# Kernel tuning notes

Measured on AMD Instinct MI355X. Metric: run time of the kernel, lower is better.

The kernel has to match this reference:

```python
import jax, jax.numpy as jnp
import numpy as np

# Multi-scale deformable attention encoder (Mask2Former pixel decoder transformer)
SHAPES = ((64, 64), (32, 32), (16, 16))  # (H, W) per level, strides 8/16/32 of 512x512
HEADS, POINTS, DM = 8, 4, 256
HD = DM // HEADS
NLVL = len(SHAPES)
NLAYERS = 6
STARTS = np.concatenate([[0], np.cumsum([h * w for h, w in SHAPES])])


def layer_norm(x, g, b, eps=1e-5):
    m = x.mean(-1, keepdims=True)
    v = ((x - m) ** 2).mean(-1, keepdims=True)
    return (x - m) * jax.lax.rsqrt(v + eps) * g + b


def ref_points(B, dtype):
    # valid_ratios == 1 (masks are all-False in the module)
    pts = []
    for H, W in SHAPES:
        ys = (jnp.arange(H, dtype=dtype) + 0.5) / H
        xs = (jnp.arange(W, dtype=dtype) + 0.5) / W
        gy, gx = jnp.meshgrid(ys, xs, indexing='ij')
        pts.append(jnp.stack([gx.reshape(-1), gy.reshape(-1)], -1))
    ref = jnp.concatenate(pts, 0)  # [Q,2]
    return jnp.broadcast_to(ref[None, :, None, :], (B, ref.shape[0], NLVL, 2))


def bilinear(value, loc, H, W):
    # grid_sample(align_corners=False, padding_mode='zeros')
    # value: [B,heads,H*W,d]; loc: [B,Q,heads,P,2] normalized to [0,1]
    x = loc[..., 0] * W - 0.5
    y = loc[..., 1] * H - 0.5
    x0f = jnp.floor(x); y0f = jnp.floor(y)
    lx = x - x0f; ly = y - y0f
    x0 = x0f.astype(jnp.int32); y0 = y0f.astype(jnp.int32)
    out = 0.
    for dx, dy, w in ((0, 0, (1 - lx) * (1 - ly)), (1, 0, lx * (1 - ly)),
                      (0, 1, (1 - lx) * ly), (1, 1, lx * ly)):
        xi = x0 + dx; yi = y0 + dy
        valid = (xi >= 0) & (xi < W) & (yi >= 0) & (yi < H)
        idx = jnp.clip(yi, 0, H - 1) * W + jnp.clip(xi, 0, W - 1)  # [B,Q,heads,P]
        idx_t = jnp.transpose(idx, (0, 2, 1, 3))  # [B,heads,Q,P]
        Bq, hq, Qq, Pq = idx_t.shape
        g = jnp.take_along_axis(value, idx_t.reshape(Bq, hq, Qq * Pq, 1), axis=2)
        g = g.reshape(Bq, hq, Qq, Pq, HD)
        wv = (w * valid).transpose(0, 2, 1, 3)[..., None]  # [B,heads,Q,P,1]
        out = out + g * wv
    return out  # [B,heads,Q,P,d]


def msda(query, src, ref, p):
    off_w, off_b, aw_w, aw_b, val_w, val_b, out_w, out_b = p
    B, Q, _ = query.shape
    value = (src @ val_w.T + val_b).reshape(B, Q, HEADS, HD).transpose(0, 2, 1, 3)  # [B,h,Q,d]
    off = (query @ off_w.T + off_b).reshape(B, Q, HEADS, NLVL, POINTS, 2)
    aw = (query @ aw_w.T + aw_b).reshape(B, Q, HEADS, NLVL * POINTS)
    aw = jax.nn.softmax(aw, -1).reshape(B, Q, HEADS, NLVL, POINTS)
    norm = jnp.array([[W, H] for H, W in SHAPES], dtype=query.dtype)  # [L,2] as (W,H)
    loc = ref[:, :, None, :, None, :] + off / norm[None, None, None, :, None, :]
    samp = []
    for l, (H, W) in enumerate(SHAPES):
        v = value[:, :, STARTS[l]:STARTS[l + 1], :]
        samp.append(bilinear(v, loc[:, :, :, l], H, W))  # [B,h,Q,P,d]
    samp = jnp.stack(samp, 3)  # [B,h,Q,L,P,d]
    w = aw.transpose(0, 2, 1, 3, 4)[..., None]  # [B,h,Q,L,P,1]
    o = (samp * w).sum((3, 4)).transpose(0, 2, 1, 3).reshape(B, Q, DM)
    return o @ out_w.T + out_b


def reference(src0, src1, src2, pos0, pos1, pos2, level_embed,
              off_w, off_b, aw_w, aw_b, val_w, val_b, out_w, out_b,
              ln1_g, ln1_b, ffn1_w, ffn1_b, ffn2_w, ffn2_b, ln2_g, ln2_b):
    srcs, poss = [src0, src1, src2], [pos0, pos1, pos2]
    B = src0.shape[0]
    xs, ps = [], []
    for l, (s, pe) in enumerate(zip(srcs, poss)):
        b, c, h, w = s.shape
        xs.append(s.reshape(b, c, h * w).transpose(0, 2, 1))
        ps.append(pe.reshape(b, c, h * w).transpose(0, 2, 1) + level_embed[l])
    x = jnp.concatenate(xs, 1)    # [B,Q,C]
    pos = jnp.concatenate(ps, 1)  # [B,Q,C]
    ref = ref_points(B, x.dtype)
    for i in range(NLAYERS):
        q = x + pos
        attn = msda(q, x, ref, (off_w[i], off_b[i], aw_w[i], aw_b[i],
                                val_w[i], val_b[i], out_w[i], out_b[i]))
        x = layer_norm(x + attn, ln1_g[i], ln1_b[i])
        h = jax.nn.relu(x @ ffn1_w[i].T + ffn1_b[i])
        x = layer_norm(x + h @ ffn2_w[i].T + ffn2_b[i], ln2_g[i], ln2_b[i])
    return x  # memory [B,Q,C]


def setup_inputs() -> dict:
    key = jax.random.key(0)
    ks = jax.random.split(key, 16)
    s = 0.02
    inp = {}
    inp['src0'] = jax.random.normal(ks[0], (4, 256, 64, 64), jnp.float32)
    inp['src1'] = jax.random.normal(ks[1], (4, 256, 32, 32), jnp.float32)
    inp['src2'] = jax.random.normal(ks[2], (4, 256, 16, 16), jnp.float32)
    inp['pos0'] = jax.random.normal(ks[3], (4, 256, 64, 64), jnp.float32)
    inp['pos1'] = jax.random.normal(ks[4], (4, 256, 32, 32), jnp.float32)
    inp['pos2'] = jax.random.normal(ks[5], (4, 256, 16, 16), jnp.float32)
    inp['level_embed'] = jax.random.normal(ks[6], (3, 256), jnp.float32)
    inp['off_w'] = jax.random.normal(ks[7], (6, 192, 256), jnp.float32) * s
    inp['off_b'] = jnp.zeros((6, 192), jnp.float32)
    inp['aw_w'] = jax.random.normal(ks[8], (6, 96, 256), jnp.float32) * s
    inp['aw_b'] = jnp.zeros((6, 96), jnp.float32)
    inp['val_w'] = jax.random.normal(ks[9], (6, 256, 256), jnp.float32) * s
    inp['val_b'] = jnp.zeros((6, 256), jnp.float32)
    inp['out_w'] = jax.random.normal(ks[10], (6, 256, 256), jnp.float32) * s
    inp['out_b'] = jnp.zeros((6, 256), jnp.float32)
    inp['ln1_g'] = jnp.ones((6, 256), jnp.float32)
    inp['ln1_b'] = jnp.zeros((6, 256), jnp.float32)
    inp['ffn1_w'] = jax.random.normal(ks[11], (6, 1024, 256), jnp.float32) * s
    inp['ffn1_b'] = jnp.zeros((6, 1024), jnp.float32)
    inp['ffn2_w'] = jax.random.normal(ks[12], (6, 256, 1024), jnp.float32) * s
    inp['ffn2_b'] = jnp.zeros((6, 256), jnp.float32)
    inp['ln2_g'] = jnp.ones((6, 256), jnp.float32)
    inp['ln2_b'] = jnp.zeros((6, 256), jnp.float32)
    return inp
```

## Files before the change

### kernel.cpp

```cpp
#include <hip/hip_runtime.h>
#include <hip/hip_bf16.h>
#include <math.h>

#define BB 4
#define QTOT 5376
#define DMM 256
#define NHEADS 8
#define HDIM 32
#define NPTS 4
#define NLVLS 3
#define BQ (BB*QTOT)
#define NOA 288

typedef short bf16x8 __attribute__((ext_vector_type(8)));
typedef unsigned short u16x8 __attribute__((ext_vector_type(8)));
typedef float f32x4  __attribute__((ext_vector_type(4)));

__device__ __forceinline__ unsigned short f2b(float f) {
  unsigned int u = __float_as_uint(f);
  unsigned int r = (u + 0x7FFFu + ((u >> 16) & 1u)) >> 16;
  return (unsigned short)r;
}
__device__ __forceinline__ float b2f(unsigned short u) {
  return __uint_as_float(((unsigned int)u) << 16);
}
__device__ __forceinline__ ushort4 f2b4(float4 v) {
  ushort4 o; o.x = f2b(v.x); o.y = f2b(v.y); o.z = f2b(v.z); o.w = f2b(v.w);
  return o;
}

__device__ __forceinline__ void gload16(const void* g, void* l) {
  __builtin_amdgcn_global_load_lds(
      (const __attribute__((address_space(1))) void*)g,
      (__attribute__((address_space(3))) void*)l, 16, 0, 0);
}

__global__ __launch_bounds__(256) void transpose_in(
    const float* __restrict__ src, const float* __restrict__ emb,
    float* __restrict__ dst, int HW, int qstart)
{
  __shared__ float t[32][33];
  int hw0 = blockIdx.x * 32, c0 = blockIdx.y * 32, b = blockIdx.z;
  int tx = threadIdx.x, ty = threadIdx.y;
  const float* s = src + ((size_t)b * DMM + c0) * HW + hw0;
#pragma unroll
  for (int j = 0; j < 4; j++)
    t[ty * 4 + j][tx] = s[(size_t)(ty * 4 + j) * HW + tx];
  __syncthreads();
  float e = emb ? emb[c0 + tx] : 0.0f;
  float* d = dst + ((size_t)b * QTOT + qstart + hw0) * DMM + c0;
#pragma unroll
  for (int j = 0; j < 4; j++)
    d[(size_t)(ty * 4 + j) * DMM + tx] = t[tx][ty * 4 + j] + e;
}

__global__ __launch_bounds__(256) void conv_b(
    const float* __restrict__ s, unsigned short* __restrict__ d, int n4)
{
  int i = blockIdx.x * 256 + threadIdx.x;
  if (i >= n4) return;
  ((ushort4*)d)[i] = f2b4(((const float4*)s)[i]);
}

__global__ __launch_bounds__(256) void pack_oa(
    const float* __restrict__ offw, const float* __restrict__ aww,
    unsigned short* __restrict__ dst)
{
  int i = blockIdx.x * 256 + threadIdx.x;
  if (i >= 6 * NOA * 64) return;
  int c4 = i & 63;
  int row = (i >> 6) % NOA;
  int l = i / (NOA * 64);
  const float* src = (row < 192)
      ? offw + ((size_t)l * 192 + row) * 256
      : aww  + ((size_t)l * 96 + (row - 192)) * 256;
  float4 v = ((const float4*)src)[c4];
  ((ushort4*)dst)[i] = f2b4(v);
}

__global__ __launch_bounds__(256) void pack_oa_bias(
    const float* __restrict__ offb, const float* __restrict__ awb,
    float* __restrict__ dst)
{
  int i = blockIdx.x * 256 + threadIdx.x;
  if (i >= 6 * NOA) return;
  int row = i % NOA, l = i / NOA;
  dst[i] = (row < 192) ? offb[l * 192 + row] : awb[l * 96 + (row - 192)];
}

__global__ __launch_bounds__(256) void prep(
    const float* __restrict__ x, const float* __restrict__ pos,
    unsigned short* __restrict__ xb, unsigned short* __restrict__ qb,
    unsigned short* __restrict__ pos16, int n4)
{
  int i = blockIdx.x * 256 + threadIdx.x;
  if (i >= n4) return;
  float4 a = ((const float4*)x)[i];
  float4 p = ((const float4*)pos)[i];
  ((ushort4*)xb)[i] = f2b4(a);
  ((ushort4*)pos16)[i] = f2b4(p);
  float4 q = make_float4(a.x + p.x, a.y + p.y, a.z + p.z, a.w + p.w);
  ((ushort4*)qb)[i] = f2b4(q);
}

__device__ __forceinline__ void gemm_tile_body(
    const unsigned short* __restrict__ A, const unsigned short* __restrict__ W,
    int m0, int n0, int K,
    unsigned short (*As)[32], unsigned short (*Ws)[32], f32x4 acc[4][4])
{
  int tid = threadIdx.x;
  int wave = tid >> 6, lane = tid & 63;
  int lr = lane & 15;
  int lkr = ((lane >> 4) ^ (lane & 3)) * 8;
  int wrr = (wave >> 1) * 64;
  int wcc = (wave & 1) * 64;

  int srow = lane >> 2;
  int schunk = ((lane & 3) ^ (srow & 3)) * 8;
  const unsigned short* Ag = A + (size_t)(m0 + wave * 32 + srow) * K + schunk;
  const unsigned short* Wg = W + (size_t)(n0 + wave * 32 + srow) * K + schunk;

#define STAGE_BF(k0, buf)                                                      \
  { int bo = (buf) * 128 + wave * 32;                                          \
    gload16(Ag + (k0), &As[bo][0]);                                            \
    gload16(Ag + (size_t)16 * K + (k0), &As[bo + 16][0]);                      \
    gload16(Wg + (k0), &Ws[bo][0]);                                            \
    gload16(Wg + (size_t)16 * K + (k0), &Ws[bo + 16][0]); }

  STAGE_BF(0, 0);
  __syncthreads();
  int cur = 0;
  for (int k0 = 0; k0 < K; k0 += 32) {
    if (k0 + 32 < K) STAGE_BF(k0 + 32, cur ^ 1);
    int bo = cur * 128;
    bf16x8 af[4], bfv[4];
#pragma unroll
    for (int m = 0; m < 4; m++)
      af[m] = *(const bf16x8*)&As[bo + wrr + m * 16 + lr][lkr];
#pragma unroll
    for (int n = 0; n < 4; n++)
      bfv[n] = *(const bf16x8*)&Ws[bo + wcc + n * 16 + lr][lkr];
#pragma unroll
    for (int m = 0; m < 4; m++)
#pragma unroll
      for (int n = 0; n < 4; n++)
        acc[m][n] = __builtin_amdgcn_mfma_f32_16x16x32_bf16(af[m], bfv[n], acc[m][n], 0, 0, 0);
    __syncthreads();
    cur ^= 1;
  }
#undef STAGE_BF
}

__device__ __forceinline__ void gemm_epilogue(
    const float* __restrict__ bias, void* __restrict__ Cout,
    int m0, int n0, int N, int relu, int bfout, f32x4 acc[4][4])
{
  int tid = threadIdx.x;
  int wave = tid >> 6, lane = tid & 63;
  int lr = lane & 15;
  int wrr = (wave >> 1) * 64;
  int wcc = (wave & 1) * 64;
  float* C32 = (float*)Cout;
  unsigned short* C16 = (unsigned short*)Cout;
#pragma unroll
  for (int n = 0; n < 4; n++) {
    int col = n0 + wcc + n * 16 + lr;
    if (col >= N) continue;
    float bv = bias[col];
#pragma unroll
    for (int m = 0; m < 4; m++) {
      int row0 = m0 + wrr + m * 16 + (lane >> 4) * 4;
#pragma unroll
      for (int j = 0; j < 4; j++) {
        float v = acc[m][n][j] + bv;
        if (relu) v = fmaxf(v, 0.0f);
        if (bfout) C16[(size_t)(row0 + j) * N + col] = f2b(v);
        else       C32[(size_t)(row0 + j) * N + col] = v;
      }
    }
  }
}

__global__ __launch_bounds__(256) void gemm_bf(
    const unsigned short* __restrict__ A, const unsigned short* __restrict__ W,
    const float* __restrict__ bias, void* __restrict__ Cout,
    int M, int N, int K, int flags)
{
  __shared__ unsigned short As[256][32];
  __shared__ unsigned short Ws[256][32];
  f32x4 acc[4][4] = {};
  int m0 = blockIdx.x * 128, n0 = blockIdx.y * 128;
  gemm_tile_body(A, W, m0, n0, K, As, Ws, acc);
  gemm_epilogue(bias, Cout, m0, n0, N, flags & 1, flags & 2, acc);
}

__global__ __launch_bounds__(256) void gemm_valoa(
    const unsigned short* __restrict__ xb, const unsigned short* __restrict__ qb,
    const unsigned short* __restrict__ vW, const unsigned short* __restrict__ oaW,
    const float* __restrict__ vBias, const float* __restrict__ oaBias,
    unsigned short* __restrict__ valb16, unsigned short* __restrict__ offaw16)
{
  __shared__ unsigned short As[256][32];
  __shared__ unsigned short Ws[256][32];
  f32x4 acc[4][4] = {};
  int m0 = blockIdx.x * 128;
  int by = blockIdx.y;
  const int K = 256;
  if (by < 2) {
    int n0 = by * 128;
    gemm_tile_body(xb, vW, m0, n0, K, As, Ws, acc);
    gemm_epilogue(vBias, valb16, m0, n0, 256, 0, 2, acc);
  } else {
    int n0 = (by - 2) * 128;
    gemm_tile_body(qb, oaW, m0, n0, K, As, Ws, acc);
    gemm_epilogue(oaBias, offaw16, m0, n0, NOA, 0, 2, acc);
  }
}

__global__ __launch_bounds__(512) void gemm_ln(
    const unsigned short* __restrict__ A, const unsigned short* __restrict__ W,
    const float* __restrict__ bias, const float* __restrict__ g,
    const float* __restrict__ beta, float* __restrict__ x,
    unsigned short* __restrict__ xb, const unsigned short* __restrict__ pos16,
    unsigned short* __restrict__ qb, int K)
{
  __shared__ unsigned short As[64][32];
  __shared__ unsigned short Ws[512][32];

  int m0 = blockIdx.x * 32;
  int tid = threadIdx.x;
  int wave = tid >> 6, lane = tid & 63;
  int lr = lane & 15;
  int lkr = ((lane >> 4) ^ (lane & 3)) * 8;
  int srow = lane >> 2;
  int schunk = ((lane & 3) ^ (srow & 3)) * 8;

  const unsigned short* Ag = A + (size_t)(m0 + (wave & 1) * 16 + srow) * K + schunk;
  const unsigned short* Wg = W + (size_t)(wave * 32 + srow) * K + schunk;

#define STAGE_LN(k0, buf)                                                      \
  { if (wave < 2) gload16(Ag + (k0), &As[(buf) * 32 + wave * 16][0]);          \
    gload16(Wg + (k0),                  &Ws[(buf) * 256 + wave * 32][0]);      \
    gload16(Wg + (size_t)16 * K + (k0), &Ws[(buf) * 256 + wave * 32 + 16][0]); }

  f32x4 acc[2][2] = {};

  STAGE_LN(0, 0);
  __syncthreads();
  int cur = 0;
  for (int k0 = 0; k0 < K; k0 += 32) {
    if (k0 + 32 < K) STAGE_LN(k0 + 32, cur ^ 1);
    bf16x8 af[2], bfv[2];
#pragma unroll
    for (int m = 0; m < 2; m++)
      af[m] = *(const bf16x8*)&As[cur * 32 + m * 16 + lr][lkr];
#pragma unroll
    for (int n = 0; n < 2; n++)
      bfv[n] = *(const bf16x8*)&Ws[cur * 256 + wave * 32 + n * 16 + lr][lkr];
#pragma unroll
    for (int m = 0; m < 2; m++)
#pragma unroll
      for (int n = 0; n < 2; n++)
        acc[m][n] = __builtin_amdgcn_mfma_f32_16x16x32_bf16(af[m], bfv[n], acc[m][n], 0, 0, 0);
    __syncthreads();
    cur ^= 1;
  }
#undef STAGE_LN

#pragma unroll
  for (int n = 0; n < 2; n++) {
    int col = wave * 32 + n * 16 + lr;
    float bv = bias[col];
#pragma unroll
    for (int m = 0; m < 2; m++) {
      int grow = m0 + m * 16 + (lane >> 4) * 4;
#pragma unroll
      for (int j = 0; j < 4; j++)
        acc[m][n][j] += bv + x[(size_t)(grow + j) * DMM + col];
    }
  }

  float2* red = (float2*)&As[0][0];
#pragma unroll
  for (int m = 0; m < 2; m++) {
#pragma unroll
    for (int j = 0; j < 4; j++) {
      float s  = acc[m][0][j] + acc[m][1][j];
      float s2 = acc[m][0][j] * acc[m][0][j] + acc[m][1][j] * acc[m][1][j];
#pragma unroll
      for (int o = 1; o < 16; o <<= 1) {
        s  += __shfl_xor(s,  o, 64);
        s2 += __shfl_xor(s2, o, 64);
      }
      if (lr == 0)
        red[(m * 16 + (lane >> 4) * 4 + j) * 8 + wave] = make_float2(s, s2);
    }
  }
  __syncthreads();

#pragma unroll
  for (int m = 0; m < 2; m++) {
#pragma unroll
    for (int j = 0; j < 4; j++) {
      int rl = m * 16 + (lane >> 4) * 4 + j;
      float ts = 0.f, ts2 = 0.f;
#pragma unroll
      for (int wv = 0; wv < 8; wv++) {
        float2 r = red[rl * 8 + wv];
        ts += r.x; ts2 += r.y;
      }
      float mean = ts * (1.0f / DMM);
      float var  = ts2 * (1.0f / DMM) - mean * mean;
      float sc = rsqrtf(var + 1e-5f);
      int grow = m0 + rl;
#pragma unroll
      for (int n = 0; n < 2; n++) {
        int col = wave * 32 + n * 16 + lr;
        float o = (acc[m][n][j] - mean) * sc * g[col] + beta[col];
        size_t idx = (size_t)grow * DMM + col;
        x[idx]  = o;
        xb[idx] = f2b(o);
        if (qb) qb[idx] = f2b(o + b2f(pos16[idx]));
      }
    }
  }
}

__global__ __launch_bounds__(256) void msda_sample(
    const unsigned short* __restrict__ value, const unsigned short* __restrict__ offaw16,
    unsigned short* __restrict__ attn16)
{
  __shared__ float saw[8][96];
  __shared__ float smx[64], sinv[64];
  __shared__ float swgt[768 * 4];
  __shared__ int   sofs[768 * 4];

  int tid = threadIdx.x;
  int qi = tid >> 5, t32 = tid & 31;
  int h = t32 >> 2, dg = t32 & 3;
  int bq0 = blockIdx.x * 8;
  int bq = bq0 + qi;
  int b = bq / QTOT;

  for (int i = t32; i < 96; i += 32)
    saw[qi][i] = b2f(offaw16[(size_t)bq * NOA + 192 + i]);
  __syncthreads();

  if (tid < 64) {
    int q2 = tid >> 3, h2 = tid & 7;
    float mx = -1e30f;
#pragma unroll
    for (int t = 0; t < 12; t++) mx = fmaxf(mx, saw[q2][h2 * 12 + t]);
    float den = 0.f;
#pragma unroll
    for (int t = 0; t < 12; t++) den += __expf(saw[q2][h2 * 12 + t] - mx);
    smx[tid] = mx;
    sinv[tid] = 1.0f / den;
  }
  __syncthreads();

  for (int s = tid; s < 768; s += 256) {
    int p = s >> 6;
    int qh = s & 63;
    int q2 = qh >> 3, h2 = qh & 7;
    int l = p >> 2;
    int Wl = 64 >> l;
    int st = (l == 0) ? 0 : ((l == 1) ? 4096 : 5120);

    int q = (bq0 + q2) % QTOT;
    int qq, Wq;
    if (q < 4096)      { qq = q;        Wq = 64; }
    else if (q < 5120) { qq = q - 4096; Wq = 32; }
    else               { qq = q - 5120; Wq = 16; }
    float refx = ((qq % Wq) + 0.5f) / Wq;
    float refy = ((qq / Wq) + 0.5f) / Wq;

    int oi = ((h2 * NLVLS + l) * NPTS + (p & 3)) * 2;
    ushort2 ob = *(const ushort2*)&offaw16[(size_t)(bq0 + q2) * NOA + oi];
    float offx = b2f(ob.x), offy = b2f(ob.y);
    float invW = 1.0f / (float)Wl;
    float xf = (refx + offx * invW) * Wl - 0.5f;
    float yf = (refy + offy * invW) * Wl - 0.5f;
    float x0f = floorf(xf), y0f = floorf(yf);
    float fx = xf - x0f, fy = yf - y0f;
    int x0 = (int)x0f, y0 = (int)y0f;

    float aw = __expf(saw[q2][h2 * 12 + p] - smx[qh]) * sinv[qh];
    float w00 = (1.f - fx) * (1.f - fy) * aw;
    float w10 = fx * (1.f - fy) * aw;
    float w01 = (1.f - fx) * fy * aw;
    float w11 = fx * fy * aw;

    bool xv0 = (x0 >= 0) & (x0 < Wl);
    bool xv1 = (x0 + 1 >= 0) & (x0 + 1 < Wl);
    bool yv0 = (y0 >= 0) & (y0 < Wl);
    bool yv1 = (y0 + 1 >= 0) & (y0 + 1 < Wl);

    int base = s * 4;
    swgt[base + 0] = (xv0 & yv0) ? w00 : 0.f;
    swgt[base + 1] = (xv1 & yv0) ? w10 : 0.f;
    swgt[base + 2] = (xv0 & yv1) ? w01 : 0.f;
    swgt[base + 3] = (xv1 & yv1) ? w11 : 0.f;
    sofs[base + 0] = (xv0 & yv0) ? (st + y0 * Wl + x0) * (DMM * 2) : 0;
    sofs[base + 1] = (xv1 & yv0) ? (st + y0 * Wl + x0 + 1) * (DMM * 2) : 0;
    sofs[base + 2] = (xv0 & yv1) ? (st + (y0 + 1) * Wl + x0) * (DMM * 2) : 0;
    sofs[base + 3] = (xv1 & yv1) ? (st + (y0 + 1) * Wl + x0 + 1) * (DMM * 2) : 0;
  }
  __syncthreads();

  float a8[8];
#pragma unroll
  for (int k = 0; k < 8; k++) a8[k] = 0.f;
  const char* vbase = (const char*)(value + (size_t)b * QTOT * DMM + h * HDIM + dg * 8);
#pragma unroll
  for (int p = 0; p < 12; p++) {
    int s3 = (p * 64 + qi * 8 + h) * 4;
    float4 w = *(const float4*)&swgt[s3];
    int4  of = *(const int4*)&sofs[s3];
    u16x8 g0 = *(const u16x8*)(vbase + of.x);
    u16x8 g1 = *(const u16x8*)(vbase + of.y);
    u16x8 g2 = *(const u16x8*)(vbase + of.z);
    u16x8 g3 = *(const u16x8*)(vbase + of.w);
#pragma unroll
    for (int k = 0; k < 8; k++)
      a8[k] += w.x * b2f((unsigned short)g0[k]) + w.y * b2f((unsigned short)g1[k])
             + w.z * b2f((unsigned short)g2[k]) + w.w * b2f((unsigned short)g3[k]);
  }
  u16x8 o;
#pragma unroll
  for (int k = 0; k < 8; k++) o[k] = f2b(a8[k]);
  *(u16x8*)(attn16 + (size_t)bq * DMM + h * HDIM + dg * 8) = o;
}

extern "C" void kernel_launch(void* const* d_in, const int* in_sizes, int n_in,
                              void* d_out, int out_size, void* d_ws, size_t ws_size,
                              hipStream_t stream)
{
  const float* src[3] = {(const float*)d_in[0], (const float*)d_in[1], (const float*)d_in[2]};
  const float* pin[3] = {(const float*)d_in[3], (const float*)d_in[4], (const float*)d_in[5]};
  const float* lvl_emb = (const float*)d_in[6];
  const float* off_w = (const float*)d_in[7];
  const float* off_b = (const float*)d_in[8];
  const float* aw_w  = (const float*)d_in[9];
  const float* aw_b  = (const float*)d_in[10];
  const float* val_w = (const float*)d_in[11];
  const float* val_b = (const float*)d_in[12];
  const float* out_w = (const float*)d_in[13];
  const float* out_b = (const float*)d_in[14];
  const float* ln1_g = (const float*)d_in[15];
  const float* ln1_b = (const float*)d_in[16];
  const float* ffn1_w = (const float*)d_in[17];
  const float* ffn1_b = (const float*)d_in[18];
  const float* ffn2_w = (const float*)d_in[19];
  const float* ffn2_b = (const float*)d_in[20];
  const float* ln2_g = (const float*)d_in[21];
  const float* ln2_b = (const float*)d_in[22];

  float* x = (float*)d_out;

  char* wsp = (char*)d_ws;
  unsigned short* offaw16 = (unsigned short*)wsp; wsp += (size_t)BQ * NOA * 2;
  unsigned short* valb16  = (unsigned short*)wsp; wsp += (size_t)BQ * 256 * 2;
  unsigned short* attnb   = (unsigned short*)wsp; wsp += (size_t)BQ * 256 * 2;
  unsigned short* hb = offaw16;
  wsp += (size_t)10 * 1024 * 1024;
  float* posb = (float*)wsp;  wsp += (size_t)BQ * 256 * 4;
  unsigned short* pos16 = (unsigned short*)wsp; wsp += (size_t)BQ * 256 * 2;
  unsigned short* xb = (unsigned short*)wsp; wsp += (size_t)BQ * 256 * 2;
  unsigned short* qb = (unsigned short*)wsp; wsp += (size_t)BQ * 256 * 2;

  unsigned short* vWb  = (unsigned short*)wsp; wsp += (size_t)6 * 256 * 256 * 2;
  unsigned short* oaWb = (unsigned short*)wsp; wsp += (size_t)6 * NOA * 256 * 2;
  unsigned short* uWb  = (unsigned short*)wsp; wsp += (size_t)6 * 256 * 256 * 2;
  unsigned short* f1Wb = (unsigned short*)wsp; wsp += (size_t)6 * 1024 * 256 * 2;
  unsigned short* f2Wb = (unsigned short*)wsp; wsp += (size_t)6 * 256 * 1024 * 2;
  float* oaBias = (float*)wsp; wsp += (size_t)6 * NOA * 4;
  wsp += 65536;

  conv_b<<<(6 * 65536 / 4 + 255) / 256, 256, 0, stream>>>(val_w, vWb, 6 * 65536 / 4);
  conv_b<<<(6 * 65536 / 4 + 255) / 256, 256, 0, stream>>>(out_w, uWb, 6 * 65536 / 4);
  conv_b<<<(6 * 262144 / 4 + 255) / 256, 256, 0, stream>>>(ffn1_w, f1Wb, 6 * 262144 / 4);
  conv_b<<<(6 * 262144 / 4 + 255) / 256, 256, 0, stream>>>(ffn2_w, f2Wb, 6 * 262144 / 4);
  pack_oa<<<(6 * NOA * 64 + 255) / 256, 256, 0, stream>>>(off_w, aw_w, oaWb);
  pack_oa_bias<<<(6 * NOA + 255) / 256, 256, 0, stream>>>(off_b, aw_b, oaBias);

  const int HWs[3] = {4096, 1024, 256};
  const int starts[3] = {0, 4096, 5120};
  for (int l = 0; l < 3; l++) {
    dim3 g(HWs[l] / 32, DMM / 32, BB), blk(32, 8);
    transpose_in<<<g, blk, 0, stream>>>(src[l], nullptr, x, HWs[l], starts[l]);
    transpose_in<<<g, blk, 0, stream>>>(pin[l], lvl_emb + l * 256, posb, HWs[l], starts[l]);
  }
  prep<<<(BQ * 256 / 4 + 255) / 256, 256, 0, stream>>>(x, posb, xb, qb, pos16, BQ * 256 / 4);

  for (int i = 0; i < 6; i++) {
    gemm_valoa<<<dim3(BQ / 128, 5), 256, 0, stream>>>(
        xb, qb, vWb + (size_t)i * 65536, oaWb + (size_t)i * NOA * 256,
        val_b + i * 256, oaBias + i * NOA, valb16, offaw16);
    msda_sample<<<BQ / 8, 256, 0, stream>>>(valb16, offaw16, attnb);
    gemm_ln<<<BQ / 32, 512, 0, stream>>>(attnb, uWb + (size_t)i * 65536,
        out_b + i * 256, ln1_g + i * 256, ln1_b + i * 256, x, xb,
        nullptr, nullptr, 256);
    gemm_bf<<<dim3(BQ / 128, 8), 256, 0, stream>>>(xb, f1Wb + (size_t)i * 262144,
        ffn1_b + i * 1024, hb, BQ, 1024, 256, 1 | 2);
    gemm_ln<<<BQ / 32, 512, 0, stream>>>(hb, f2Wb + (size_t)i * 262144,
        ffn2_b + i * 256, ln2_g + i * 256, ln2_b + i * 256, x, xb,
        pos16, qb, 1024);
  }
}
```

Before: 933.3 us.

## Load weight fragments directly to registers in gemm_ln, stage only activations in LDS

Reworks the gemm_ln main loop so each wave reads its own weight fragments straight from global memory into registers, prefetched one k-step ahead. Only the small activation tile still goes through LDS, now register-staged into a padded double buffer instead of using gload16 with XOR swizzling. This shrinks LDS use (the 512x32 weight buffer is gone, and the reduction scratch gets its own array) and drops LDS traffic for weights, which could raise occupancy. In exchange, the per-lane global weight loads are narrower and less coalesced, and waits are now handled with explicit waitcnt and barriers.

Result: slower. 1.058 ms (+13.3%).

```diff
diff --git a/kernel.cpp b/kernel.cpp
--- a/kernel.cpp
+++ b/kernel.cpp
@@ -224,48 +224,58 @@
     unsigned short* __restrict__ xb, const unsigned short* __restrict__ pos16,
     unsigned short* __restrict__ qb, int K)
 {
-  __shared__ unsigned short As[64][32];
-  __shared__ unsigned short Ws[512][32];
+  __shared__ unsigned short As[2][32][40];
+  __shared__ float2 red[32 * 8];
 
   int m0 = blockIdx.x * 32;
   int tid = threadIdx.x;
   int wave = tid >> 6, lane = tid & 63;
   int lr = lane & 15;
-  int lkr = ((lane >> 4) ^ (lane & 3)) * 8;
-  int srow = lane >> 2;
-  int schunk = ((lane & 3) ^ (srow & 3)) * 8;
-
-  const unsigned short* Ag = A + (size_t)(m0 + (wave & 1) * 16 + srow) * K + schunk;
-  const unsigned short* Wg = W + (size_t)(wave * 32 + srow) * K + schunk;
-
-#define STAGE_LN(k0, buf)                                                      \
-  { if (wave < 2) gload16(Ag + (k0), &As[(buf) * 32 + wave * 16][0]);          \
-    gload16(Wg + (k0),                  &Ws[(buf) * 256 + wave * 32][0]);      \
-    gload16(Wg + (size_t)16 * K + (k0), &Ws[(buf) * 256 + wave * 32 + 16][0]); }
+  int p4 = lane >> 4;
+
+  bool stg = wave < 2;
+  int srow = wave * 16 + (lane >> 2);
+  int sch = (lane & 3) * 8;
+  const unsigned short* Ag = A + (size_t)(m0 + srow) * K + sch;
+
+  const unsigned short* Wg0 = W + (size_t)(wave * 32 + lr) * K + p4 * 8;
+  const unsigned short* Wg1 = W + (size_t)(wave * 32 + 16 + lr) * K + p4 * 8;
 
   f32x4 acc[2][2] = {};
-
-  STAGE_LN(0, 0);
-  __syncthreads();
+  int nst = K >> 5;
+
+  u16x8 a_nx = {};
+  if (stg) a_nx = *(const u16x8*)(Ag);
+  bf16x8 wn0 = *(const bf16x8*)(Wg0);
+  bf16x8 wn1 = *(const bf16x8*)(Wg1);
+  if (stg) *(u16x8*)&As[0][srow][sch] = a_nx;
+  asm volatile("s_waitcnt lgkmcnt(0)" ::: "memory");
+  __builtin_amdgcn_s_barrier();
+  __builtin_amdgcn_sched_barrier(0);
+
   int cur = 0;
-  for (int k0 = 0; k0 < K; k0 += 32) {
-    if (k0 + 32 < K) STAGE_LN(k0 + 32, cur ^ 1);
-    bf16x8 af[2], bfv[2];
-#pragma unroll
-    for (int m = 0; m < 2; m++)
-      af[m] = *(const bf16x8*)&As[cur * 32 + m * 16 + lr][lkr];
-#pragma unroll
-    for (int n = 0; n < 2; n++)
-      bfv[n] = *(const bf16x8*)&Ws[cur * 256 + wave * 32 + n * 16 + lr][lkr];
-#pragma unroll
-    for (int m = 0; m < 2; m++)
-#pragma unroll
-      for (int n = 0; n < 2; n++)
-        acc[m][n] = __builtin_amdgcn_mfma_f32_16x16x32_bf16(af[m], bfv[n], acc[m][n], 0, 0, 0);
-    __syncthreads();
+  for (int t = 0; t < nst; ++t) {
+    bf16x8 wm0, wm1; u16x8 aa = {};
+    if (t + 1 < nst) {
+      if (stg) aa = *(const u16x8*)(Ag + (size_t)(t + 1) * 32);
+      wm0 = *(const bf16x8*)(Wg0 + (size_t)(t + 1) * 32);
+      wm1 = *(const bf16x8*)(Wg1 + (size_t)(t + 1) * 32);
+    }
+    bf16x8 af0 = *(const bf16x8*)&As[cur][lr][p4 * 8];
+    bf16x8 af1 = *(const bf16x8*)&As[cur][16 + lr][p4 * 8];
+    acc[0][0] = __builtin_amdgcn_mfma_f32_16x16x32_bf16(af0, wn0, acc[0][0], 0, 0, 0);
+    acc[0][1] = __builtin_amdgcn_mfma_f32_16x16x32_bf16(af0, wn1, acc[0][1], 0, 0, 0);
+    acc[1][0] = __builtin_amdgcn_mfma_f32_16x16x32_bf16(af1, wn0, acc[1][0], 0, 0, 0);
+    acc[1][1] = __builtin_amdgcn_mfma_f32_16x16x32_bf16(af1, wn1, acc[1][1], 0, 0, 0);
+    if (t + 1 < nst) {
+      if (stg) *(u16x8*)&As[cur ^ 1][srow][sch] = aa;
+      wn0 = wm0; wn1 = wm1;
+    }
+    asm volatile("s_waitcnt lgkmcnt(0)" ::: "memory");
+    __builtin_amdgcn_s_barrier();
+    __builtin_amdgcn_sched_barrier(0);
     cur ^= 1;
   }
-#undef STAGE_LN
 
 #pragma unroll
   for (int n = 0; n < 2; n++) {
@@ -273,14 +283,13 @@
     float bv = bias[col];
 #pragma unroll
     for (int m = 0; m < 2; m++) {
-      int grow = m0 + m * 16 + (lane >> 4) * 4;
+      int grow = m0 + m * 16 + p4 * 4;
 #pragma unroll
       for (int j = 0; j < 4; j++)
         acc[m][n][j] += bv + x[(size_t)(grow + j) * DMM + col];
     }
   }
 
-  float2* red = (float2*)&As[0][0];
 #pragma unroll
   for (int m = 0; m < 2; m++) {
 #pragma unroll
@@ -293,7 +302,7 @@
         s2 += __shfl_xor(s2, o, 64);
       }
       if (lr == 0)
-        red[(m * 16 + (lane >> 4) * 4 + j) * 8 + wave] = make_float2(s, s2);
+        red[(m * 16 + p4 * 4 + j) * 8 + wave] = make_float2(s, s2);
     }
   }
   __syncthreads();
@@ -302,7 +311,7 @@
   for (int m = 0; m < 2; m++) {
 #pragma unroll
     for (int j = 0; j < 4; j++) {
-      int rl = m * 16 + (lane >> 4) * 4 + j;
+      int rl = m * 16 + p4 * 4 + j;
       float ts = 0.f, ts2 = 0.f;
 #pragma unroll
       for (int wv = 0; wv < 8; wv++) {
```
